# Kernel tuning notes

Hardware: AMD Instinct MI355X
Metric: run time of the kernel (lower is better)

## Reference

```python
import jax, jax.numpy as jnp
import numpy as np

B, F = 512, 512
K, D = 32, 16  # num_kernels, dim_per_kernel


def setup_inputs() -> dict:
    key = jax.random.key(0)
    kx, kt = jax.random.split(key)
    x = jax.random.normal(kx, (B, F), dtype=jnp.float32)
    # keras 'uniform' init is small-range uniform; scale similarly
    T = jax.random.uniform(kt, (F, K * D), dtype=jnp.float32, minval=-0.05, maxval=0.05)
    return {"x": x, "T": T}


def reference(x, T):
    # m: [B, K, D]
    m = (x @ T).reshape(-1, K, D)
    # all-pairs L1 distance per kernel: [B, B, K]
    abs_diffs = jnp.sum(jnp.abs(m[:, None, :, :] - m[None, :, :, :]), axis=-1)
    # minibatch features: sum_j exp(-||m_i - m_j||_1) -> [B, K]
    feats = jnp.sum(jnp.exp(-abs_diffs), axis=1)
    return jnp.concatenate([x, feats], axis=1)
```

## Files before the change

### kernel.cpp

```cpp
#include <hip/hip_runtime.h>
#include <hip/hip_bf16.h>
#include <math.h>

#define BSZ 512
#define FDIM 512
#define NK 32
#define DD 16
#define NDIM (NK*DD)
#define OUTW (FDIM + NK)

typedef __attribute__((ext_vector_type(8))) short short8;
typedef __attribute__((ext_vector_type(4))) float float4v;

static __device__ __forceinline__ short f2bf(float f) {
  return (short)__builtin_bit_cast(unsigned short, __float2bfloat16(f));
}

__global__ __launch_bounds__(256) void k_gemm(
    const float* __restrict__ x, const float* __restrict__ T,
    float* __restrict__ m, float* __restrict__ out) {
  const int t  = threadIdx.x;
  const int b  = blockIdx.x;
  const int rg = b >> 5, cg = b & 31;
  const int r0 = rg * 16, c0 = cg * 16;
  const int lane = t & 63;
  const int w    = __builtin_amdgcn_readfirstlane(t >> 6);
  const int mi   = lane & 15;
  const int q    = lane >> 4;

  const float* __restrict__ xa = x + (size_t)(r0 + mi) * FDIM + 128 * w + 8 * q;
  const float* __restrict__ tb = T + (size_t)(128 * w + 8 * q) * NDIM + c0 + mi;

  float4v acc = {0.f, 0.f, 0.f, 0.f};
#pragma unroll
  for (int j = 0; j < 4; ++j) {
    const float4 a0 = *(const float4*)(xa + 32 * j);
    const float4 a1 = *(const float4*)(xa + 32 * j + 4);
    float bv[8];
#pragma unroll
    for (int i = 0; i < 8; ++i) bv[i] = tb[(size_t)(32 * j + i) * NDIM];
    short8 af, bf;
    af[0] = f2bf(a0.x); af[1] = f2bf(a0.y); af[2] = f2bf(a0.z); af[3] = f2bf(a0.w);
    af[4] = f2bf(a1.x); af[5] = f2bf(a1.y); af[6] = f2bf(a1.z); af[7] = f2bf(a1.w);
#pragma unroll
    for (int i = 0; i < 8; ++i) bf[i] = f2bf(bv[i]);
    acc = __builtin_amdgcn_mfma_f32_16x16x32_bf16(af, bf, acc, 0, 0, 0);
  }

  __shared__ float red[4][16][16];
#pragma unroll
  for (int r = 0; r < 4; ++r) red[w][q * 4 + r][mi] = acc[r];
  __syncthreads();
  {
    const int orow = t >> 4, ocol = t & 15;
    const float s = red[0][orow][ocol] + red[1][orow][ocol] +
                    red[2][orow][ocol] + red[3][orow][ocol];
    m[(size_t)(r0 + orow) * NDIM + c0 + ocol] = s;
  }

  const int g = b * 256 + t;
  if (g < 65536) {
    const int orow = g >> 7, c4 = g & 127;
    *(float4*)(out + (size_t)orow * OUTW + c4 * 4) =
        *(const float4*)(x + (size_t)orow * FDIM + c4 * 4);
  } else if (g < 65536 + 16384) {
    const int idx = g - 65536;
    const int orow = idx >> 5, kk = idx & 31;
    out[(size_t)orow * OUTW + FDIM + kk] = 0.f;
  }
}

__global__ __launch_bounds__(256) void k_dist(
    const float* __restrict__ m, float* __restrict__ out) {
  __shared__ float Bs[128 * DD];
  __shared__ float red[256];
  const int t   = threadIdx.x;
  const int bid = blockIdx.x;
  const int ig  = bid >> 7;
  const int k   = (bid >> 2) & 31;
  const int jq  = bid & 3;
  const int lane = t & 63;
  const int i    = ig * 64 + lane;

  const float4* ap = (const float4*)(m + (size_t)i * NDIM + k * DD);
  const float4 A0 = ap[0], A1 = ap[1], A2 = ap[2], A3 = ap[3];

  const float* mb = m + (size_t)(jq * 128) * NDIM + k * DD;
#pragma unroll
  for (int qq = 0; qq < 2; ++qq) {
    const int idx = qq * 256 + t;
    const int jrow = idx >> 2, part = idx & 3;
    *(float4*)&Bs[jrow * DD + part * 4] =
        *(const float4*)(mb + (size_t)jrow * NDIM + part * 4);
  }
  __syncthreads();

  float a[DD];
  a[0]=A0.x; a[1]=A0.y; a[2]=A0.z;  a[3]=A0.w;
  a[4]=A1.x; a[5]=A1.y; a[6]=A1.z;  a[7]=A1.w;
  a[8]=A2.x; a[9]=A2.y; a[10]=A2.z; a[11]=A2.w;
  a[12]=A3.x;a[13]=A3.y;a[14]=A3.z; a[15]=A3.w;

  const int w = __builtin_amdgcn_readfirstlane(t >> 6);
  const int jbase = w * 32;
  float f = 0.f;
#pragma unroll 4
  for (int j = 0; j < 32; ++j) {
    const float4* bp = (const float4*)&Bs[(jbase + j) * DD];
    const float4 b0 = bp[0], b1 = bp[1], b2 = bp[2], b3 = bp[3];
    float d =
        fabsf(a[0]  - b0.x) + fabsf(a[1]  - b0.y) +
        fabsf(a[2]  - b0.z) + fabsf(a[3]  - b0.w) +
        fabsf(a[4]  - b1.x) + fabsf(a[5]  - b1.y) +
        fabsf(a[6]  - b1.z) + fabsf(a[7]  - b1.w) +
        fabsf(a[8]  - b2.x) + fabsf(a[9]  - b2.y) +
        fabsf(a[10] - b2.z) + fabsf(a[11] - b2.w) +
        fabsf(a[12] - b3.x) + fabsf(a[13] - b3.y) +
        fabsf(a[14] - b3.z) + fabsf(a[15] - b3.w);
    f += __expf(-d);
  }

  red[t] = f;
  __syncthreads();
  if (t < 64) {
    const float s = red[t] + red[t + 64] + red[t + 128] + red[t + 192];
    atomicAdd(out + (size_t)(ig * 64 + t) * OUTW + FDIM + k, s);
  }
}

extern "C" void kernel_launch(void* const* d_in, const int* in_sizes, int n_in,
                              void* d_out, int out_size, void* d_ws,
                              size_t ws_size, hipStream_t stream) {
  (void)in_sizes; (void)n_in; (void)out_size; (void)ws_size;
  const float* x = (const float*)d_in[0];
  const float* T = (const float*)d_in[1];
  float* out = (float*)d_out;
  float* m   = (float*)d_ws;

  hipLaunchKernelGGL(k_gemm, dim3(1024), dim3(256), 0, stream, x, T, m, out);
  hipLaunchKernelGGL(k_dist, dim3(1024), dim3(256), 0, stream, m, out);
}
```

Before: 72.34 us.

## Pre-convert x and transposed T to bf16, split GEMM into prep and MFMA kernels

```diff
diff --git a/kernel.cpp b/kernel.cpp
--- a/kernel.cpp
+++ b/kernel.cpp
@@ -11,63 +11,80 @@
 
 typedef __attribute__((ext_vector_type(8))) short short8;
 typedef __attribute__((ext_vector_type(4))) float float4v;
+typedef __attribute__((ext_vector_type(4))) unsigned short ushort4v;
 
-static __device__ __forceinline__ short f2bf(float f) {
-  return (short)__builtin_bit_cast(unsigned short, __float2bfloat16(f));
+static __device__ __forceinline__ unsigned short f2bf(float f) {
+  return __builtin_bit_cast(unsigned short, __float2bfloat16(f));
 }
 
-__global__ __launch_bounds__(256) void k_gemm(
+
+__global__ __launch_bounds__(256) void k_prep(
     const float* __restrict__ x, const float* __restrict__ T,
-    float* __restrict__ m, float* __restrict__ out) {
-  const int t  = threadIdx.x;
-  const int b  = blockIdx.x;
-  const int rg = b >> 5, cg = b & 31;
-  const int r0 = rg * 16, c0 = cg * 16;
+    unsigned short* __restrict__ xb, unsigned short* __restrict__ Tb,
+    float* __restrict__ out) {
+  const int t = threadIdx.x;
+  const int b = blockIdx.x;
+
+  if (b < 256) {
+    const int g = b * 256 + t;
+    const int row = g >> 7, c4 = g & 127;
+    const float4 v = *(const float4*)(x + (size_t)row * FDIM + c4 * 4);
+    ushort4v o;
+    o.x = f2bf(v.x); o.y = f2bf(v.y); o.z = f2bf(v.z); o.w = f2bf(v.w);
+    *(ushort4v*)(xb + (size_t)row * FDIM + c4 * 4) = o;
+  } else if (b < 768) {
+    const int row = b - 256;
+    if (t < 136) {
+      float4 v;
+      if (t < 128) v = *(const float4*)(x + (size_t)row * FDIM + t * 4);
+      else         v = make_float4(0.f, 0.f, 0.f, 0.f);
+      *(float4*)(out + (size_t)row * OUTW + t * 4) = v;
+    }
+  } else {
+    __shared__ float s[32][33];
+    const int tb = b - 768;
+    const int k0 = (tb >> 4) * 32, c0 = (tb & 15) * 32;
+    const int cc = t & 31, kq = t >> 5;
+#pragma unroll
+    for (int u = 0; u < 4; ++u) {
+      const int kl = u * 8 + kq;
+      s[kl][cc] = T[(size_t)(k0 + kl) * NDIM + c0 + cc];
+    }
+    __syncthreads();
+    const int cl = t >> 3, kg = t & 7;
+    ushort4v o;
+    o.x = f2bf(s[kg * 4 + 0][cl]); o.y = f2bf(s[kg * 4 + 1][cl]);
+    o.z = f2bf(s[kg * 4 + 2][cl]); o.w = f2bf(s[kg * 4 + 3][cl]);
+    *(ushort4v*)(Tb + (size_t)(c0 + cl) * NDIM + k0 + kg * 4) = o;
+  }
+}
+
+__global__ __launch_bounds__(256) void k_mm(
+    const unsigned short* __restrict__ xb,
+    const unsigned short* __restrict__ Tb, float* __restrict__ m) {
+  const int t = threadIdx.x;
+  const int b = blockIdx.x;
+  const int r0 = (b >> 4) * 32, c0 = (b & 15) * 32;
   const int lane = t & 63;
-  const int w    = __builtin_amdgcn_readfirstlane(t >> 6);
-  const int mi   = lane & 15;
-  const int q    = lane >> 4;
+  const int w  = __builtin_amdgcn_readfirstlane(t >> 6);
+  const int wr = w >> 1, wc = w & 1;
+  const int mi = lane & 15;
+  const int q  = lane >> 4;
 
-  const float* __restrict__ xa = x + (size_t)(r0 + mi) * FDIM + 128 * w + 8 * q;
-  const float* __restrict__ tb = T + (size_t)(128 * w + 8 * q) * NDIM + c0 + mi;
+  const unsigned short* pa = xb + (size_t)(r0 + 16 * wr + mi) * FDIM + 8 * q;
+  const unsigned short* pb = Tb + (size_t)(c0 + 16 * wc + mi) * NDIM + 8 * q;
 
   float4v acc = {0.f, 0.f, 0.f, 0.f};
 #pragma unroll
-  for (int j = 0; j < 4; ++j) {
-    const float4 a0 = *(const float4*)(xa + 32 * j);
-    const float4 a1 = *(const float4*)(xa + 32 * j + 4);
-    float bv[8];
-#pragma unroll
-    for (int i = 0; i < 8; ++i) bv[i] = tb[(size_t)(32 * j + i) * NDIM];
-    short8 af, bf;
-    af[0] = f2bf(a0.x); af[1] = f2bf(a0.y); af[2] = f2bf(a0.z); af[3] = f2bf(a0.w);
-    af[4] = f2bf(a1.x); af[5] = f2bf(a1.y); af[6] = f2bf(a1.z); af[7] = f2bf(a1.w);
-#pragma unroll
-    for (int i = 0; i < 8; ++i) bf[i] = f2bf(bv[i]);
+  for (int kk = 0; kk < 16; ++kk) {
+    const short8 af = *(const short8*)(pa + 32 * kk);
+    const short8 bf = *(const short8*)(pb + 32 * kk);
     acc = __builtin_amdgcn_mfma_f32_16x16x32_bf16(af, bf, acc, 0, 0, 0);
   }
 
-  __shared__ float red[4][16][16];
+  float* mo = m + (size_t)(r0 + 16 * wr + 4 * q) * NDIM + c0 + 16 * wc + mi;
 #pragma unroll
-  for (int r = 0; r < 4; ++r) red[w][q * 4 + r][mi] = acc[r];
-  __syncthreads();
-  {
-    const int orow = t >> 4, ocol = t & 15;
-    const float s = red[0][orow][ocol] + red[1][orow][ocol] +
-                    red[2][orow][ocol] + red[3][orow][ocol];
-    m[(size_t)(r0 + orow) * NDIM + c0 + ocol] = s;
-  }
-
-  const int g = b * 256 + t;
-  if (g < 65536) {
-    const int orow = g >> 7, c4 = g & 127;
-    *(float4*)(out + (size_t)orow * OUTW + c4 * 4) =
-        *(const float4*)(x + (size_t)orow * FDIM + c4 * 4);
-  } else if (g < 65536 + 16384) {
-    const int idx = g - 65536;
-    const int orow = idx >> 5, kk = idx & 31;
-    out[(size_t)orow * OUTW + FDIM + kk] = 0.f;
-  }
+  for (int r = 0; r < 4; ++r) mo[(size_t)r * NDIM] = acc[r];
 }
 
 __global__ __launch_bounds__(256) void k_dist(
@@ -135,8 +152,11 @@
   const float* x = (const float*)d_in[0];
   const float* T = (const float*)d_in[1];
   float* out = (float*)d_out;
-  float* m   = (float*)d_ws;
+  unsigned short* xb = (unsigned short*)d_ws;
+  unsigned short* Tb = (unsigned short*)((char*)d_ws + (512 << 10));
+  float* m           = (float*)((char*)d_ws + (1 << 20));
 
-  hipLaunchKernelGGL(k_gemm, dim3(1024), dim3(256), 0, stream, x, T, m, out);
+  hipLaunchKernelGGL(k_prep, dim3(1024), dim3(256), 0, stream, x, T, xb, Tb, out);
+  hipLaunchKernelGGL(k_mm,   dim3(256),  dim3(256), 0, stream, xb, Tb, m);
   hipLaunchKernelGGL(k_dist, dim3(1024), dim3(256), 0, stream, m, out);
 }
```

After: 73.52 us. Within noise of the previous version (+1.6%).

## Retile GEMM to 32x32 blocks with full-K per wave, split copy into separate blocks

Applied to the files above, without the earlier changes.

```diff
diff --git a/kernel.cpp b/kernel.cpp
--- a/kernel.cpp
+++ b/kernel.cpp
@@ -16,57 +16,51 @@
   return (short)__builtin_bit_cast(unsigned short, __float2bfloat16(f));
 }
 
-__global__ __launch_bounds__(256) void k_gemm(
+
+__global__ __launch_bounds__(256) void k1(
     const float* __restrict__ x, const float* __restrict__ T,
     float* __restrict__ m, float* __restrict__ out) {
-  const int t  = threadIdx.x;
-  const int b  = blockIdx.x;
-  const int rg = b >> 5, cg = b & 31;
-  const int r0 = rg * 16, c0 = cg * 16;
-  const int lane = t & 63;
-  const int w    = __builtin_amdgcn_readfirstlane(t >> 6);
-  const int mi   = lane & 15;
-  const int q    = lane >> 4;
+  const int t = threadIdx.x;
+  const int b = blockIdx.x;
 
-  const float* __restrict__ xa = x + (size_t)(r0 + mi) * FDIM + 128 * w + 8 * q;
-  const float* __restrict__ tb = T + (size_t)(128 * w + 8 * q) * NDIM + c0 + mi;
+  if (b < 256) {
+    const int r0 = (b >> 4) * 32, c0 = (b & 15) * 32;
+    const int lane = t & 63;
+    const int w  = __builtin_amdgcn_readfirstlane(t >> 6);
+    const int wr = w >> 1, wc = w & 1;
+    const int mi = lane & 15;
+    const int q  = lane >> 4;
 
-  float4v acc = {0.f, 0.f, 0.f, 0.f};
+    const float* __restrict__ pa = x + (size_t)(r0 + 16 * wr + mi) * FDIM + 8 * q;
+    const float* __restrict__ pb = T + (size_t)(8 * q) * NDIM + c0 + 16 * wc + mi;
+
+    float4v acc = {0.f, 0.f, 0.f, 0.f};
 #pragma unroll
-  for (int j = 0; j < 4; ++j) {
-    const float4 a0 = *(const float4*)(xa + 32 * j);
-    const float4 a1 = *(const float4*)(xa + 32 * j + 4);
-    float bv[8];
+    for (int kk = 0; kk < 16; ++kk) {
+      const float4 a0 = *(const float4*)(pa + 32 * kk);
+      const float4 a1 = *(const float4*)(pa + 32 * kk + 4);
+      float bv[8];
 #pragma unroll
-    for (int i = 0; i < 8; ++i) bv[i] = tb[(size_t)(32 * j + i) * NDIM];
-    short8 af, bf;
-    af[0] = f2bf(a0.x); af[1] = f2bf(a0.y); af[2] = f2bf(a0.z); af[3] = f2bf(a0.w);
-    af[4] = f2bf(a1.x); af[5] = f2bf(a1.y); af[6] = f2bf(a1.z); af[7] = f2bf(a1.w);
+      for (int i = 0; i < 8; ++i) bv[i] = pb[(size_t)(32 * kk + i) * NDIM];
+      short8 af, bf;
+      af[0] = f2bf(a0.x); af[1] = f2bf(a0.y); af[2] = f2bf(a0.z); af[3] = f2bf(a0.w);
+      af[4] = f2bf(a1.x); af[5] = f2bf(a1.y); af[6] = f2bf(a1.z); af[7] = f2bf(a1.w);
 #pragma unroll
-    for (int i = 0; i < 8; ++i) bf[i] = f2bf(bv[i]);
-    acc = __builtin_amdgcn_mfma_f32_16x16x32_bf16(af, bf, acc, 0, 0, 0);
-  }
+      for (int i = 0; i < 8; ++i) bf[i] = f2bf(bv[i]);
+      acc = __builtin_amdgcn_mfma_f32_16x16x32_bf16(af, bf, acc, 0, 0, 0);
+    }
 
-  __shared__ float red[4][16][16];
+    float* mo = m + (size_t)(r0 + 16 * wr + 4 * q) * NDIM + c0 + 16 * wc + mi;
 #pragma unroll
-  for (int r = 0; r < 4; ++r) red[w][q * 4 + r][mi] = acc[r];
-  __syncthreads();
-  {
-    const int orow = t >> 4, ocol = t & 15;
-    const float s = red[0][orow][ocol] + red[1][orow][ocol] +
-                    red[2][orow][ocol] + red[3][orow][ocol];
-    m[(size_t)(r0 + orow) * NDIM + c0 + ocol] = s;
-  }
-
-  const int g = b * 256 + t;
-  if (g < 65536) {
-    const int orow = g >> 7, c4 = g & 127;
-    *(float4*)(out + (size_t)orow * OUTW + c4 * 4) =
-        *(const float4*)(x + (size_t)orow * FDIM + c4 * 4);
-  } else if (g < 65536 + 16384) {
-    const int idx = g - 65536;
-    const int orow = idx >> 5, kk = idx & 31;
-    out[(size_t)orow * OUTW + FDIM + kk] = 0.f;
+    for (int r = 0; r < 4; ++r) mo[(size_t)r * NDIM] = acc[r];
+  } else {
+    const int row = b - 256;
+    if (t < 136) {
+      float4 v;
+      if (t < 128) v = *(const float4*)(x + (size_t)row * FDIM + t * 4);
+      else         v = make_float4(0.f, 0.f, 0.f, 0.f);
+      *(float4*)(out + (size_t)row * OUTW + t * 4) = v;
+    }
   }
 }
 
@@ -137,6 +131,6 @@
   float* out = (float*)d_out;
   float* m   = (float*)d_ws;
 
-  hipLaunchKernelGGL(k_gemm, dim3(1024), dim3(256), 0, stream, x, T, m, out);
+  hipLaunchKernelGGL(k1,     dim3(768),  dim3(256), 0, stream, x, T, m, out);
   hipLaunchKernelGGL(k_dist, dim3(1024), dim3(256), 0, stream, m, out);
 }
```

Measured after the change: 72.66 us. Within noise of the previous version (+0.4%).
